# Optimization experiments

Hardware: AMD Instinct MI355X
Metric: run time of the kernel (lower is better)

Reference implementation:

```python
import jax, jax.numpy as jnp
import numpy as np

N_IN = 2048
N_OUT = 2048
RANK = 64
NUM_ITER = 4  # Newton-Schulz iterations, matches default num_iter=4


def setup_inputs() -> dict:
    key = jax.random.key(0)
    k1, k2, k3 = jax.random.split(key, 3)
    # scale U,V modestly so A = UV^T - VU^T is well-conditioned (mimics orthogonal init scale)
    scale = 1.0 / np.sqrt(N_IN)
    return {
        "input": jax.random.normal(k1, (8, 2048, N_IN), dtype=jnp.float32),
        "U": jax.random.normal(k2, (N_IN, RANK), dtype=jnp.float32) * scale,
        "V": jax.random.normal(k3, (N_IN, RANK), dtype=jnp.float32) * scale,
    }


def _orthogonal_weight(U, V):
    # A = U V^T - V U^T  (skew-symmetric, rank <= 2*rank)
    A = U @ V.T - V @ U.T              # [n, n]
    I = jnp.eye(N_IN, dtype=A.dtype)
    B = I - A
    X = I
    for _ in range(NUM_ITER):          # Newton-Schulz iteration for B^{-1}
        X = X @ (2.0 * I - B @ X)
    W_square = (I + A) @ X             # Cayley transform (I+A)(I-A)^{-1} approx
    return W_square[:N_OUT, :N_IN]


def reference(input, U, V):
    W = _orthogonal_weight(U, V)       # [out, in]
    # F.linear(input, W) = input @ W.T
    return jnp.einsum("bsi,oi->bso", input, W)
```

## Files before the change

kernel.cpp:

```cpp
#include <hip/hip_runtime.h>
#include <hip/hip_bf16.h>
#include <cstdint>
#include <cstddef>

#define NIN   2048
#define RANK  64
#define R2    128
#define NROWS 16384

typedef __bf16 bf16x8 __attribute__((ext_vector_type(8)));
typedef float  f32x4  __attribute__((ext_vector_type(4)));
typedef unsigned short u16x8 __attribute__((ext_vector_type(8)));

__device__ __forceinline__ unsigned short f2bf(float f) {
  union { float f; unsigned u; } x; x.f = f;
  return (unsigned short)((x.u + 0x7fffu + ((x.u >> 16) & 1u)) >> 16);
}

__device__ __forceinline__ void smallGemm(const float* __restrict__ A,
                                          const float* __restrict__ B,
                                          float* __restrict__ O,
                                          float a, float b, int t, int tid) {
  int i = (t >> 3) * 16 + (tid >> 4);
  int j = (t & 7) * 16 + (tid & 15);
  float acc = 0.f;
#pragma unroll 8
  for (int k = 0; k < R2; ++k) {
    float av = A[i * R2 + k]; if (k == i) av += a;
    float bv = B[k * R2 + j]; if (k == j) bv += b;
    acc += av * bv;
  }
  O[i * R2 + j] = acc;
}

__global__ __launch_bounds__(512) void k_prep(const float* __restrict__ U,
                                              const float* __restrict__ V,
                                              unsigned short* __restrict__ Mf,
                                              unsigned short* __restrict__ Mrf,
                                              float* __restrict__ G) {
  __shared__ float red[512];
  int b = blockIdx.x, tid = threadIdx.x;
  if (b < 64) {
    int CI = b * 512 + tid;
    int lane = CI & 63, J = (CI >> 6) & 63, t = CI >> 12;
    int n = t * 16 + (lane & 15);
    int k0 = J * 32 + (lane >> 4) * 8;
    const float* src = (n < RANK) ? (U + n) : (V + (n - RANK));
    u16x8 h;
#pragma unroll
    for (int e = 0; e < 8; ++e) h[e] = f2bf(src[(size_t)(k0 + e) * RANK]);
    *(u16x8*)(Mf + (size_t)CI * 8) = h;
  } else if (b < 128) {
    int tile = b - 64;
    int bi = tile >> 3, bj = tile & 7;
    int sub = tid >> 8, t256 = tid & 255;
    int ty = t256 >> 4, tx = t256 & 15;
    int i = bi * 16 + ty, j = bj * 16 + tx;
    const float* Ai = (i < RANK) ? (U + i) : (V + (i - RANK));
    const float* Aj = (j < RANK) ? (U + j) : (V + (j - RANK));
    int k0 = sub * 1024;
    float p0 = 0.f, p1 = 0.f, p2 = 0.f, p3 = 0.f;
#pragma unroll 4
    for (int k = k0; k < k0 + 1024; k += 4) {
      p0 += Ai[(size_t)k * RANK]       * Aj[(size_t)k * RANK];
      p1 += Ai[(size_t)(k + 1) * RANK] * Aj[(size_t)(k + 1) * RANK];
      p2 += Ai[(size_t)(k + 2) * RANK] * Aj[(size_t)(k + 2) * RANK];
      p3 += Ai[(size_t)(k + 3) * RANK] * Aj[(size_t)(k + 3) * RANK];
    }
    red[tid] = (p0 + p1) + (p2 + p3);
    __syncthreads();
    if (sub == 0) {
      float s = red[t256] + red[256 + t256];
      if (i < RANK) G[(i + RANK) * R2 + j] = -s;
      else          G[(i - RANK) * R2 + j] =  s;
    }
  } else {
    int CI = (b - 128) * 512 + tid;
    int lane = CI & 63, rest = CI >> 6;
    int lr = lane & 15, lg = lane >> 4;
    int J = rest & 3, t_ = rest >> 2;
    int i = t_ * 16 + lr, j0 = J * 32 + lg * 8;
    const float* src = (j0 < RANK) ? (U + (size_t)i * RANK + j0)
                                   : (V + (size_t)i * RANK + (j0 - RANK));
    float4 f0 = *(const float4*)src, f1 = *(const float4*)(src + 4);
    u16x8 h;
    h[0] = f2bf(f0.x); h[1] = f2bf(f0.y); h[2] = f2bf(f0.z); h[3] = f2bf(f0.w);
    h[4] = f2bf(f1.x); h[5] = f2bf(f1.y); h[6] = f2bf(f1.z); h[7] = f2bf(f1.w);
    *(u16x8*)(Mrf + (size_t)CI * 8) = h;
  }
}

struct SOp { const float* A; const float* B; float* O; float a, b; };
struct SOps { SOp op[3]; };
__global__ void k_small(SOps ops) {
  SOp o = ops.op[blockIdx.x >> 6];
  smallGemm(o.A, o.B, o.O, o.a, o.b, blockIdx.x & 63, threadIdx.x);
}

__global__ __launch_bounds__(256) void k_T1(const float* __restrict__ input,
                                            const unsigned short* __restrict__ Mf,
                                            unsigned short* __restrict__ T1bf,
                                            const float* __restrict__ G,
                                            float* __restrict__ G2) {
  __shared__ __align__(16) unsigned char lds[36864];
  if (blockIdx.x >= 512) {
    smallGemm(G, G, G2, 0.f, 0.f, blockIdx.x - 512, threadIdx.x);
    return;
  }
  const int tid = threadIdx.x, lane = tid & 63, w = tid >> 6;
  const int lr = lane & 15, lg = lane >> 4;
  const int row0 = blockIdx.x * 32;
  unsigned char* abuf = lds + w * 8192;

  f32x4 acc[2][8] = {};
  const float* gbase = input + (size_t)row0 * NIN + w * 512;
  const int Jbase = w * 16;
  float4 s0[8], s1[8];
  bf16x8 bx[8], by[8];

#define T1_SLOAD(KT)                                                          \
  _Pragma("unroll") for (int p = 0; p < 8; ++p) {                             \
    int id = p * 64 + lane; int r = id >> 4, C = id & 15;                     \
    const float* g = gbase + (size_t)r * NIN + (KT) * 128 + C * 8;            \
    s0[p] = *(const float4*)g; s1[p] = *(const float4*)(g + 4);               \
  }
#define T1_SWRITE()                                                           \
  _Pragma("unroll") for (int p = 0; p < 8; ++p) {                             \
    int id = p * 64 + lane; int r = id >> 4, C = id & 15;                     \
    u16x8 h;                                                                  \
    h[0] = f2bf(s0[p].x); h[1] = f2bf(s0[p].y);                               \
    h[2] = f2bf(s0[p].z); h[3] = f2bf(s0[p].w);                               \
    h[4] = f2bf(s1[p].x); h[5] = f2bf(s1[p].y);                               \
    h[6] = f2bf(s1[p].z); h[7] = f2bf(s1[p].w);                               \
    *(u16x8*)(abuf + r * 256 + ((C ^ (r & 7)) << 4)) = h;                     \
  }
#define T1_BLOAD(P, S)                                                        \
  _Pragma("unroll") for (int t = 0; t < 8; ++t)                               \
    P[t] = *(const bf16x8*)(Mf + ((size_t)(t * 64 + Jbase + (S)) * 64 + lane) * 8);

  T1_SLOAD(0);
  T1_SWRITE();
  T1_BLOAD(bx, 0);
#pragma unroll
  for (int s = 0; s < 16; ++s) {
    const int kt = s >> 2, j = s & 3;
    if (j == 0 && kt < 3) { T1_SLOAD(kt + 1); }
    bf16x8 a0, a1;
    {
      int C = j * 4 + lg;
      a0 = *(const bf16x8*)(abuf + lr * 256 + ((C ^ (lr & 7)) << 4));
      a1 = *(const bf16x8*)(abuf + (16 + lr) * 256 + ((C ^ ((16 + lr) & 7)) << 4));
    }
    if (s < 15) { if (s & 1) { T1_BLOAD(bx, s + 1); } else { T1_BLOAD(by, s + 1); } }
#pragma unroll
    for (int t = 0; t < 8; ++t) {
      bf16x8 bcur = (s & 1) ? by[t] : bx[t];
      acc[0][t] = __builtin_amdgcn_mfma_f32_16x16x32_bf16(a0, bcur, acc[0][t], 0, 0, 0);
      acc[1][t] = __builtin_amdgcn_mfma_f32_16x16x32_bf16(a1, bcur, acc[1][t], 0, 0, 0);
    }
    if (j == 3 && kt < 3) { T1_SWRITE(); }
  }

  float* rbw = (float*)lds + (size_t)w * 2304;
#pragma unroll
  for (int m = 0; m < 2; ++m) {
    __syncthreads();
#pragma unroll
    for (int t = 0; t < 8; ++t) {
      int col = t * 16 + lr;
#pragma unroll
      for (int e = 0; e < 4; ++e) rbw[(lg * 4 + e) * 128 + col] = acc[m][t][e];
    }
    __syncthreads();
    {
      int r = tid >> 4, cg = tid & 15;
      f32x4 a0 = {}, a1 = {};
#pragma unroll
      for (int ww = 0; ww < 4; ++ww) {
        const float* p = (const float*)lds + (size_t)ww * 2304 + r * 128 + cg * 8;
        a0 += *(const f32x4*)p;
        a1 += *(const f32x4*)(p + 4);
      }
      u16x8 o;
#pragma unroll
      for (int i = 0; i < 4; ++i) { o[i] = f2bf(a0[i]); o[4 + i] = f2bf(a1[i]); }
      *(u16x8*)(T1bf + (size_t)(row0 + m * 16 + r) * R2 + cg * 8) = o;
    }
  }
}

__global__ __launch_bounds__(256) void k_OUT(const float* __restrict__ input,
                                             const unsigned short* __restrict__ T1bf,
                                             const float* __restrict__ Hm,
                                             const float* __restrict__ G15m,
                                             const unsigned short* __restrict__ Mrf,
                                             float* __restrict__ out) {
  __shared__ __align__(16) unsigned char lds[43008];
  unsigned char* cbuf = lds;
  unsigned char* t2buf = lds + 34816;
  const int tid = threadIdx.x, lane = tid & 63, w = tid >> 6;
  const int lr = lane & 15, lg = lane >> 4;
  const int row0 = blockIdx.x * 32;

#pragma unroll
  for (int it = 0; it < 8; ++it) {
    int id = it * 256 + tid;
    int k = id >> 4, j8 = id & 15, j0 = j8 * 8;
    int jj0 = (j0 < RANK) ? j0 + RANK : j0 - RANK;
    float sgn = (j0 < RANK) ? -1.f : 1.f;
    const float* hp = Hm + k * R2 + jj0;
    const float* gp = G15m + k * R2 + jj0;
    float4 h0 = *(const float4*)hp, h1 = *(const float4*)(hp + 4);
    float4 g0 = *(const float4*)gp, g1 = *(const float4*)(gp + 4);
    u16x8 cv;
    cv[0] = f2bf(sgn * (2.f * h0.x - g0.x));
    cv[1] = f2bf(sgn * (2.f * h0.y - g0.y));
    cv[2] = f2bf(sgn * (2.f * h0.z - g0.z));
    cv[3] = f2bf(sgn * (2.f * h0.w - g0.w));
    cv[4] = f2bf(sgn * (2.f * h1.x - g1.x));
    cv[5] = f2bf(sgn * (2.f * h1.y - g1.y));
    cv[6] = f2bf(sgn * (2.f * h1.z - g1.z));
    cv[7] = f2bf(sgn * (2.f * h1.w - g1.w));
    *(u16x8*)(cbuf + k * 256 + ((j8 ^ (k & 7)) << 4)) = cv;
  }
  bf16x8 t1f[2][4];
#pragma unroll
  for (int R = 0; R < 2; ++R)
#pragma unroll
    for (int J = 0; J < 4; ++J)
      t1f[R][J] = *(const bf16x8*)(T1bf + (size_t)(row0 + R * 16 + lr) * R2 + J * 32 + lg * 8);
  __syncthreads();

#pragma unroll
  for (int kk = 0; kk < 2; ++kk) {
    int kct = w * 2 + kk;
    int kc = kct * 16 + lr;
    f32x4 a2[2] = {};
#pragma unroll
    for (int jkt = 0; jkt < 4; ++jkt) {
      bf16x8 cf = *(const bf16x8*)(cbuf + kc * 256 + (((jkt * 4 + lg) ^ (kc & 7)) << 4));
#pragma unroll
      for (int R = 0; R < 2; ++R)
        a2[R] = __builtin_amdgcn_mfma_f32_16x16x32_bf16(cf, t1f[R][jkt], a2[R], 0, 0, 0);
    }
#pragma unroll
    for (int R = 0; R < 2; ++R) {
      int r = R * 16 + lr;
      ushort4 p;
      p.x = f2bf(a2[R][0]); p.y = f2bf(a2[R][1]);
      p.z = f2bf(a2[R][2]); p.w = f2bf(a2[R][3]);
      int gran = kct * 2 + (lg >> 1), off = (lg & 1) * 8;
      *(ushort4*)(t2buf + r * 256 + ((gran ^ (r & 7)) << 4) + off) = p;
    }
  }
  __syncthreads();

  bf16x8 bq[2][4];
#pragma unroll
  for (int R = 0; R < 2; ++R)
#pragma unroll
    for (int J = 0; J < 4; ++J) {
      int row = R * 16 + lr;
      bq[R][J] = *(const bf16x8*)(t2buf + row * 256 + (((J * 4 + lg) ^ (row & 7)) << 4));
    }

  float* obufw = (float*)(lds + w * 8704);
  bf16x8 xd[4], yd[4];
#define O_DLOAD(P, TTI)                                                       \
  _Pragma("unroll") for (int J = 0; J < 4; ++J)                               \
    P[J] = *(const bf16x8*)(Mrf + ((size_t)((w * 32 + (TTI)) * 4 + J) * 64 + lane) * 8);

  O_DLOAD(xd, 0);
#pragma unroll
  for (int g = 0; g < 8; ++g) {
#pragma unroll
    for (int tt = 0; tt < 4; ++tt) {
      const int tti = g * 4 + tt;
      if (tti < 31) { if (tti & 1) { O_DLOAD(xd, tti + 1); } else { O_DLOAD(yd, tti + 1); } }
#pragma unroll
      for (int R = 0; R < 2; ++R) {
        f32x4 o = {};
#pragma unroll
        for (int J = 0; J < 4; ++J) {
          bf16x8 d = (tti & 1) ? yd[J] : xd[J];
          o = __builtin_amdgcn_mfma_f32_16x16x32_bf16(d, bq[R][J], o, 0, 0, 0);
        }
        *(f32x4*)&obufw[(R * 16 + lr) * 68 + tt * 16 + lg * 4] = o;
      }
    }
#pragma unroll
    for (int c = 0; c < 8; ++c) {
      int id = c * 64 + lane, r = id >> 4, cc = id & 15;
      f32x4 v = *(const f32x4*)&obufw[r * 68 + cc * 4];
      int grow = row0 + r, gcol = w * 512 + g * 64 + cc * 4;
      float4 inv = *(const float4*)(input + (size_t)grow * NIN + gcol);
      float4 res = { v[0] + inv.x, v[1] + inv.y, v[2] + inv.z, v[3] + inv.w };
      *(float4*)(out + (size_t)grow * NIN + gcol) = res;
    }
  }
}

extern "C" void kernel_launch(void* const* d_in, const int* in_sizes, int n_in,
                              void* d_out, int out_size, void* d_ws, size_t ws_size,
                              hipStream_t stream) {
  const float* input = (const float*)d_in[0];
  const float* U     = (const float*)d_in[1];
  const float* V     = (const float*)d_in[2];
  float* out = (float*)d_out;
  char* ws = (char*)d_ws;

  float* mats = (float*)ws;
  float* G   = mats + 0 * 16384;
  float* G2  = mats + 1 * 16384;
  float* G3  = mats + 2 * 16384;
  float* G4  = mats + 3 * 16384;
  float* G7  = mats + 4 * 16384;
  float* G8  = mats + 5 * 16384;
  float* H12 = mats + 6 * 16384;
  float* H124= mats + 7 * 16384;
  float* H   = mats + 8 * 16384;
  float* G15 = mats + 9 * 16384;
  unsigned short* Mf   = (unsigned short*)(ws + 10 * 65536);
  unsigned short* Mrf  = (unsigned short*)(ws + 10 * 65536 + 524288);
  unsigned short* T1bf = (unsigned short*)(ws + 10 * 65536 + 2 * 524288);

  k_prep<<<192, 512, 0, stream>>>(U, V, Mf, Mrf, G);
  k_T1<<<576, 256, 0, stream>>>(input, Mf, T1bf, G, G2);

  { SOps o = {{ {G2, G2, G4, 0.f, 0.f}, {G2, G, G3, 0.f, 0.f}, {G, G2, H12, 1.f, 1.f} }};
    k_small<<<192, 256, 0, stream>>>(o); }
  { SOps o = {{ {G4, G4, G8, 0.f, 0.f}, {G3, G4, G7, 0.f, 0.f}, {H12, G4, H124, 0.f, 1.f} }};
    k_small<<<192, 256, 0, stream>>>(o); }
  { SOps o = {{ {G7, G8, G15, 0.f, 0.f}, {H124, G8, H, 0.f, 1.f}, {nullptr,nullptr,nullptr,0.f,0.f} }};
    k_small<<<128, 256, 0, stream>>>(o); }

  k_OUT<<<512, 256, 0, stream>>>(input, T1bf, H, G15, Mrf, out);
}
```

Baseline: 137.9 us.

## Halve T1 row tile, double-buffer LDS staging, pad reduction buffer, raise occupancy

The k_T1 projection kernel now handles 16 rows per block instead of 32, so the grid doubles to 1024 GEMM blocks plus the small-GEMM tail. Each wave's LDS A-tile is double-buffered, and the next slice is written early, during the sub-step before it is consumed. The cross-wave reduction buffer is padded to a stride of 132 floats to avoid bank conflicts. Both big kernels get launch_bounds(256,3) to favour occupancy. In exchange, each B fragment is reused for fewer rows, so B-operand traffic per row doubles, and the register cap may cause spills.

After: 140.1 us. No clear change (+1.5%).

```diff
diff --git a/kernel.cpp b/kernel.cpp
--- a/kernel.cpp
+++ b/kernel.cpp
@@ -97,104 +97,95 @@
   smallGemm(o.A, o.B, o.O, o.a, o.b, blockIdx.x & 63, threadIdx.x);
 }
 
-__global__ __launch_bounds__(256) void k_T1(const float* __restrict__ input,
-                                            const unsigned short* __restrict__ Mf,
-                                            unsigned short* __restrict__ T1bf,
-                                            const float* __restrict__ G,
-                                            float* __restrict__ G2) {
-  __shared__ __align__(16) unsigned char lds[36864];
-  if (blockIdx.x >= 512) {
-    smallGemm(G, G, G2, 0.f, 0.f, blockIdx.x - 512, threadIdx.x);
+__global__ __launch_bounds__(256, 3) void k_T1(const float* __restrict__ input,
+                                               const unsigned short* __restrict__ Mf,
+                                               unsigned short* __restrict__ T1bf,
+                                               const float* __restrict__ G,
+                                               float* __restrict__ G2) {
+  __shared__ __align__(16) unsigned char lds[33792];
+  if (blockIdx.x >= 1024) {
+    smallGemm(G, G, G2, 0.f, 0.f, blockIdx.x - 1024, threadIdx.x);
     return;
   }
   const int tid = threadIdx.x, lane = tid & 63, w = tid >> 6;
   const int lr = lane & 15, lg = lane >> 4;
-  const int row0 = blockIdx.x * 32;
-  unsigned char* abuf = lds + w * 8192;
-
-  f32x4 acc[2][8] = {};
+  const int row0 = blockIdx.x * 16;
+  unsigned char* ab0 = lds + w * 8192;
+
+  f32x4 acc[8] = {};
   const float* gbase = input + (size_t)row0 * NIN + w * 512;
   const int Jbase = w * 16;
-  float4 s0[8], s1[8];
+  float4 s0[4], s1[4];
   bf16x8 bx[8], by[8];
 
 #define T1_SLOAD(KT)                                                          \
-  _Pragma("unroll") for (int p = 0; p < 8; ++p) {                             \
-    int id = p * 64 + lane; int r = id >> 4, C = id & 15;                     \
+  _Pragma("unroll") for (int c = 0; c < 4; ++c) {                             \
+    int id = c * 64 + lane; int r = id >> 4, C = id & 15;                     \
     const float* g = gbase + (size_t)r * NIN + (KT) * 128 + C * 8;            \
-    s0[p] = *(const float4*)g; s1[p] = *(const float4*)(g + 4);               \
-  }
-#define T1_SWRITE()                                                           \
-  _Pragma("unroll") for (int p = 0; p < 8; ++p) {                             \
-    int id = p * 64 + lane; int r = id >> 4, C = id & 15;                     \
+    s0[c] = *(const float4*)g; s1[c] = *(const float4*)(g + 4);               \
+  }
+#define T1_SWRITE(BUF)                                                        \
+  _Pragma("unroll") for (int c = 0; c < 4; ++c) {                             \
+    int id = c * 64 + lane; int r = id >> 4, C = id & 15;                     \
     u16x8 h;                                                                  \
-    h[0] = f2bf(s0[p].x); h[1] = f2bf(s0[p].y);                               \
-    h[2] = f2bf(s0[p].z); h[3] = f2bf(s0[p].w);                               \
-    h[4] = f2bf(s1[p].x); h[5] = f2bf(s1[p].y);                               \
-    h[6] = f2bf(s1[p].z); h[7] = f2bf(s1[p].w);                               \
-    *(u16x8*)(abuf + r * 256 + ((C ^ (r & 7)) << 4)) = h;                     \
+    h[0] = f2bf(s0[c].x); h[1] = f2bf(s0[c].y);                               \
+    h[2] = f2bf(s0[c].z); h[3] = f2bf(s0[c].w);                               \
+    h[4] = f2bf(s1[c].x); h[5] = f2bf(s1[c].y);                               \
+    h[6] = f2bf(s1[c].z); h[7] = f2bf(s1[c].w);                               \
+    *(u16x8*)(ab0 + (BUF) * 4096 + r * 256 + ((C ^ (r & 7)) << 4)) = h;       \
   }
 #define T1_BLOAD(P, S)                                                        \
   _Pragma("unroll") for (int t = 0; t < 8; ++t)                               \
     P[t] = *(const bf16x8*)(Mf + ((size_t)(t * 64 + Jbase + (S)) * 64 + lane) * 8);
 
   T1_SLOAD(0);
-  T1_SWRITE();
+  T1_SWRITE(0);
   T1_BLOAD(bx, 0);
 #pragma unroll
   for (int s = 0; s < 16; ++s) {
-    const int kt = s >> 2, j = s & 3;
-    if (j == 0 && kt < 3) { T1_SLOAD(kt + 1); }
-    bf16x8 a0, a1;
-    {
-      int C = j * 4 + lg;
-      a0 = *(const bf16x8*)(abuf + lr * 256 + ((C ^ (lr & 7)) << 4));
-      a1 = *(const bf16x8*)(abuf + (16 + lr) * 256 + ((C ^ ((16 + lr) & 7)) << 4));
-    }
+    const int kt = s >> 2, sub = s & 3, buf = kt & 1;
+    if (sub == 0 && kt < 3) { T1_SLOAD(kt + 1); }
+    bf16x8 a = *(const bf16x8*)(ab0 + buf * 4096 + lr * 256 + (((sub * 4 + lg) ^ (lr & 7)) << 4));
     if (s < 15) { if (s & 1) { T1_BLOAD(bx, s + 1); } else { T1_BLOAD(by, s + 1); } }
 #pragma unroll
     for (int t = 0; t < 8; ++t) {
       bf16x8 bcur = (s & 1) ? by[t] : bx[t];
-      acc[0][t] = __builtin_amdgcn_mfma_f32_16x16x32_bf16(a0, bcur, acc[0][t], 0, 0, 0);
-      acc[1][t] = __builtin_amdgcn_mfma_f32_16x16x32_bf16(a1, bcur, acc[1][t], 0, 0, 0);
-    }
-    if (j == 3 && kt < 3) { T1_SWRITE(); }
-  }
-
-  float* rbw = (float*)lds + (size_t)w * 2304;
-#pragma unroll
-  for (int m = 0; m < 2; ++m) {
-    __syncthreads();
-#pragma unroll
-    for (int t = 0; t < 8; ++t) {
-      int col = t * 16 + lr;
-#pragma unroll
-      for (int e = 0; e < 4; ++e) rbw[(lg * 4 + e) * 128 + col] = acc[m][t][e];
-    }
-    __syncthreads();
-    {
-      int r = tid >> 4, cg = tid & 15;
-      f32x4 a0 = {}, a1 = {};
-#pragma unroll
-      for (int ww = 0; ww < 4; ++ww) {
-        const float* p = (const float*)lds + (size_t)ww * 2304 + r * 128 + cg * 8;
-        a0 += *(const f32x4*)p;
-        a1 += *(const f32x4*)(p + 4);
-      }
-      u16x8 o;
-#pragma unroll
-      for (int i = 0; i < 4; ++i) { o[i] = f2bf(a0[i]); o[4 + i] = f2bf(a1[i]); }
-      *(u16x8*)(T1bf + (size_t)(row0 + m * 16 + r) * R2 + cg * 8) = o;
-    }
-  }
-}
-
-__global__ __launch_bounds__(256) void k_OUT(const float* __restrict__ input,
-                                             const unsigned short* __restrict__ T1bf,
-                                             const float* __restrict__ Hm,
-                                             const float* __restrict__ G15m,
-                                             const unsigned short* __restrict__ Mrf,
-                                             float* __restrict__ out) {
+      acc[t] = __builtin_amdgcn_mfma_f32_16x16x32_bf16(a, bcur, acc[t], 0, 0, 0);
+    }
+    if (sub == 2 && kt < 3) { T1_SWRITE(buf ^ 1); }
+  }
+
+  __syncthreads();
+  float* rbw = (float*)lds + (size_t)w * 2112;
+#pragma unroll
+  for (int t = 0; t < 8; ++t) {
+    int col = t * 16 + lr;
+#pragma unroll
+    for (int e = 0; e < 4; ++e) rbw[(lg * 4 + e) * 132 + col] = acc[t][e];
+  }
+  __syncthreads();
+  {
+    int r = tid >> 4, c8 = tid & 15;
+    f32x4 a0 = {}, a1 = {};
+#pragma unroll
+    for (int ww = 0; ww < 4; ++ww) {
+      const float* p = (const float*)lds + (size_t)ww * 2112 + r * 132 + c8 * 8;
+      a0 += *(const f32x4*)p;
+      a1 += *(const f32x4*)(p + 4);
+    }
+    u16x8 o;
+#pragma unroll
+    for (int i = 0; i < 4; ++i) { o[i] = f2bf(a0[i]); o[4 + i] = f2bf(a1[i]); }
+    *(u16x8*)(T1bf + (size_t)(row0 + r) * R2 + c8 * 8) = o;
+  }
+}
+
+__global__ __launch_bounds__(256, 3) void k_OUT(const float* __restrict__ input,
+                                                const unsigned short* __restrict__ T1bf,
+                                                const float* __restrict__ Hm,
+                                                const float* __restrict__ G15m,
+                                                const unsigned short* __restrict__ Mrf,
+                                                float* __restrict__ out) {
   __shared__ __align__(16) unsigned char lds[43008];
   unsigned char* cbuf = lds;
   unsigned char* t2buf = lds + 34816;
@@ -325,7 +316,7 @@
   unsigned short* T1bf = (unsigned short*)(ws + 10 * 65536 + 2 * 524288);
 
   k_prep<<<192, 512, 0, stream>>>(U, V, Mf, Mrf, G);
-  k_T1<<<576, 256, 0, stream>>>(input, Mf, T1bf, G, G2);
+  k_T1<<<1088, 256, 0, stream>>>(input, Mf, T1bf, G, G2);
 
   { SOps o = {{ {G2, G2, G4, 0.f, 0.f}, {G2, G, G3, 0.f, 0.f}, {G, G2, H12, 1.f, 1.f} }};
     k_small<<<192, 256, 0, stream>>>(o); }
```
